# Performance work log

Hardware: AMD Instinct MI355X
Metric: run time of the kernel (lower is better)

## Reference

```python
import jax, jax.numpy as jnp
import numpy as np

B, N, C_IN, C_OUT, F = 8, 2048, 256, 256, 8
EPS = 1e-4

def setup_inputs() -> dict:
    key = jax.random.key(0)
    k1, k2, k3, k4, k5 = jax.random.split(key, 5)
    node_feats = jax.random.normal(k1, (B, N, C_IN), dtype=jnp.float32)
    # sparse-ish 0/1 adjacency with self-loops already added (as module assumes)
    adj = (jax.random.uniform(k2, (B, N, N)) < 0.02).astype(jnp.float32)
    eye = jnp.eye(N, dtype=jnp.float32)[None, :, :]
    adj_matrix = jnp.maximum(adj, eye)
    filters = jax.random.normal(k3, (F, C_OUT, C_IN), dtype=jnp.float32) * (1.0 / np.sqrt(C_IN))
    proj_w = jax.random.normal(k4, (1, F), dtype=jnp.float32) * (1.0 / np.sqrt(F))
    proj_b = jax.random.normal(k5, (1,), dtype=jnp.float32) * 0.01
    return {"node_feats": node_feats, "adj_matrix": adj_matrix,
            "filters": filters, "proj_w": proj_w, "proj_b": proj_b}

def reference(node_feats, adj_matrix, filters, proj_w, proj_b):
    # Multi-head filter transform + projection over heads, fused algebraically:
    # torch: ext[b,n,k,f] = sum_i filters[f,k,i]*x[b,n,i]; x' = ext @ proj_w.T + proj_b
    x = jnp.einsum('bni,fki,f->bnk', node_feats, filters, proj_w[0]) + proj_b[0]  # [B,N,c_out]
    # adjacency-weighted aggregation + mean normalization
    num_neighbours = jnp.sum(adj_matrix, axis=-1, keepdims=True)  # [B,N,1]
    agg = jnp.einsum('bij,bjk->bik', adj_matrix, x)  # [B,N,c_out]
    return agg / (num_neighbours + EPS)
```

## Files before the change

kernel.cpp:

```cpp
#include <hip/hip_runtime.h>
#include <hip/hip_bf16.h>

#define B_DIM  8
#define N_DIM  2048
#define CIN    256
#define COUT   256
#define F_DIM  8
#define EPS    1e-4f

using short8 = __attribute__((ext_vector_type(8))) short;
using f32x4  = __attribute__((ext_vector_type(4))) float;

__device__ __forceinline__ unsigned short f2bf(float f) {
    union { float f; unsigned u; } x; x.f = f;
    unsigned r = x.u + 0x7FFFu + ((x.u >> 16) & 1u);
    return (unsigned short)(r >> 16);
}
__device__ __forceinline__ float bf2f(unsigned short u) {
    union { unsigned u; float f; } x; x.u = ((unsigned)u) << 16;
    return x.f;
}

__global__ __launch_bounds__(256) void wb_build(const float* __restrict__ filters,
                                                const float* __restrict__ proj_w,
                                                unsigned short* __restrict__ Wb) {
    int gid = blockIdx.x * 256 + threadIdx.x;
    float acc = 0.f;
#pragma unroll
    for (int f = 0; f < F_DIM; ++f)
        acc += proj_w[f] * filters[f * (COUT * CIN) + gid];
    Wb[gid] = f2bf(acc);
}

__global__ __launch_bounds__(256) void xp_gemm(const float* __restrict__ nf,
                                               const unsigned short* __restrict__ Wb,
                                               const float* __restrict__ proj_b,
                                               unsigned short* __restrict__ xp) {
    const int tid  = threadIdx.x;
    const int lane = tid & 63;
    const int wv   = tid >> 6;
    const int m0   = blockIdx.x * 64;
    const int lrow = lane & 15;
    const int kgrp = lane >> 4;
    const float bias = proj_b[0];

    f32x4 acc[4][4];
#pragma unroll
    for (int a = 0; a < 4; ++a)
#pragma unroll
        for (int b = 0; b < 4; ++b)
            acc[a][b] = (f32x4){0.f, 0.f, 0.f, 0.f};

#pragma unroll
    for (int ks = 0; ks < 8; ++ks) {
        const int klane = ks * 32 + kgrp * 8;
        short8 af[4], bfr[4];
#pragma unroll
        for (int fm = 0; fm < 4; ++fm) {
            const float* ap = nf + (size_t)(m0 + fm * 16 + lrow) * CIN + klane;
            float4 a0 = *(const float4*)ap;
            float4 a1 = *(const float4*)(ap + 4);
            short8 t;
            t[0] = (short)f2bf(a0.x); t[1] = (short)f2bf(a0.y);
            t[2] = (short)f2bf(a0.z); t[3] = (short)f2bf(a0.w);
            t[4] = (short)f2bf(a1.x); t[5] = (short)f2bf(a1.y);
            t[6] = (short)f2bf(a1.z); t[7] = (short)f2bf(a1.w);
            af[fm] = t;
        }
#pragma unroll
        for (int fn = 0; fn < 4; ++fn) {
            const unsigned short* bp =
                Wb + (size_t)(wv * 64 + fn * 16 + lrow) * CIN + klane;
            bfr[fn] = *(const short8*)bp;
        }
#pragma unroll
        for (int fm = 0; fm < 4; ++fm)
#pragma unroll
            for (int fn = 0; fn < 4; ++fn)
                acc[fm][fn] = __builtin_amdgcn_mfma_f32_16x16x32_bf16(
                    af[fm], bfr[fn], acc[fm][fn], 0, 0, 0);
    }

#pragma unroll
    for (int fm = 0; fm < 4; ++fm) {
#pragma unroll
        for (int fn = 0; fn < 4; ++fn) {
            const int gcol = wv * 64 + fn * 16 + lrow;
#pragma unroll
            for (int r = 0; r < 4; ++r) {
                const int grow = m0 + fm * 16 + kgrp * 4 + r;
                xp[(size_t)grow * COUT + gcol] = f2bf(acc[fm][fn][r] + bias);
            }
        }
    }
}

__global__ __launch_bounds__(256) void agg_sparse(const float* __restrict__ adj,
                                                  const unsigned short* __restrict__ xp,
                                                  float* __restrict__ out) {
    __shared__ int   s_idx[N_DIM];
    __shared__ float s_val[N_DIM];
    __shared__ int   s_wcnt[4];
    __shared__ float s_wdeg[4];

    const int tid  = threadIdx.x;
    const int lane = tid & 63;
    const int wid  = tid >> 6;
    const int bid  = blockIdx.x;
    const int b    = bid & 7;
    const int i    = bid >> 3;

    const float* row = adj + ((size_t)b * N_DIM + i) * N_DIM;

    const float4* r4 = (const float4*)(row + tid * 8);
    float4 va = r4[0], vb = r4[1];
    float v[8] = {va.x, va.y, va.z, va.w, vb.x, vb.y, vb.z, vb.w};

    int   c = 0;
    float dsum = 0.f;
#pragma unroll
    for (int e = 0; e < 8; ++e) { dsum += v[e]; c += (v[e] != 0.f); }

    int pre = c;
#pragma unroll
    for (int off = 1; off < 64; off <<= 1) {
        int n = __shfl_up(pre, off, 64);
        if (lane >= off) pre += n;
    }
    float ds = dsum;
#pragma unroll
    for (int off = 32; off; off >>= 1) ds += __shfl_down(ds, off, 64);
    if (lane == 63) s_wcnt[wid] = pre;
    if (lane == 0)  s_wdeg[wid] = ds;
    __syncthreads();

    int base = 0;
#pragma unroll
    for (int ww = 0; ww < 4; ++ww) if (ww < wid) base += s_wcnt[ww];
    const int   cnt = s_wcnt[0] + s_wcnt[1] + s_wcnt[2] + s_wcnt[3];
    const float deg = s_wdeg[0] + s_wdeg[1] + s_wdeg[2] + s_wdeg[3];

    int p = base + (pre - c);
#pragma unroll
    for (int e = 0; e < 8; ++e) {
        if (v[e] != 0.f) { s_idx[p] = tid * 8 + e; s_val[p] = v[e]; ++p; }
    }
    __syncthreads();

    const unsigned short* xb = xp + (size_t)b * N_DIM * COUT + tid;
    float acc = 0.f;
    int t = 0;
    for (; t + 4 <= cnt; t += 4) {
        int j0 = s_idx[t], j1 = s_idx[t + 1], j2 = s_idx[t + 2], j3 = s_idx[t + 3];
        float w0 = s_val[t], w1 = s_val[t + 1], w2 = s_val[t + 2], w3 = s_val[t + 3];
        float x0 = bf2f(xb[(size_t)j0 * COUT]);
        float x1 = bf2f(xb[(size_t)j1 * COUT]);
        float x2 = bf2f(xb[(size_t)j2 * COUT]);
        float x3 = bf2f(xb[(size_t)j3 * COUT]);
        acc += w0 * x0; acc += w1 * x1; acc += w2 * x2; acc += w3 * x3;
    }
    for (; t < cnt; ++t)
        acc += s_val[t] * bf2f(xb[(size_t)s_idx[t] * COUT]);

    out[((size_t)b * N_DIM + i) * COUT + tid] = acc / (deg + EPS);
}

extern "C" void kernel_launch(void* const* d_in, const int* in_sizes, int n_in,
                              void* d_out, int out_size, void* d_ws, size_t ws_size,
                              hipStream_t stream) {
    const float* nf      = (const float*)d_in[0];
    const float* adj     = (const float*)d_in[1];
    const float* filters = (const float*)d_in[2];
    const float* proj_w  = (const float*)d_in[3];
    const float* proj_b  = (const float*)d_in[4];
    float* out = (float*)d_out;

    unsigned short* Wb = (unsigned short*)d_ws;
    unsigned short* xp = (unsigned short*)((char*)d_ws + COUT * CIN * 2);

    wb_build<<<(COUT * CIN) / 256, 256, 0, stream>>>(filters, proj_w, Wb);
    xp_gemm<<<(B_DIM * N_DIM) / 64, 256, 0, stream>>>(nf, Wb, proj_b, xp);
    agg_sparse<<<B_DIM * N_DIM, 256, 0, stream>>>(adj, xp, out);
}
```

Baseline: 73.98 us.

## Replace sparse gather aggregation with dense bf16 MFMA adjacency GEMM

The sparse per-row compaction and gather is replaced by a dense MFMA GEMM that multiplies the adjacency (truncated to bf16, exact for 0/1 values) by a transposed projected feature matrix, computing degrees on the fly. The feature GEMM is reoriented to write x' transposed so B-operand loads are contiguous. This removes the irregular gathers and shared-memory compaction, but performs dense work and launches only 256 blocks, which may limit memory-level parallelism when streaming the large adjacency. Truncating adjacency to bf16 assumes exactly representable values.

```diff
diff --git a/kernel.cpp b/kernel.cpp
--- a/kernel.cpp
+++ b/kernel.cpp
@@ -7,6 +7,7 @@
 #define COUT   256
 #define F_DIM  8
 #define EPS    1e-4f
+#define MTOT   (B_DIM * N_DIM)
 
 using short8 = __attribute__((ext_vector_type(8))) short;
 using f32x4  = __attribute__((ext_vector_type(4))) float;
@@ -16,9 +17,9 @@
     unsigned r = x.u + 0x7FFFu + ((x.u >> 16) & 1u);
     return (unsigned short)(r >> 16);
 }
-__device__ __forceinline__ float bf2f(unsigned short u) {
-    union { unsigned u; float f; } x; x.u = ((unsigned)u) << 16;
-    return x.f;
+__device__ __forceinline__ unsigned fbits(float f) {
+    union { float f; unsigned u; } x; x.f = f;
+    return x.u;
 }
 
 __global__ __launch_bounds__(256) void wb_build(const float* __restrict__ filters,
@@ -32,16 +33,17 @@
     Wb[gid] = f2bf(acc);
 }
 
-__global__ __launch_bounds__(256) void xp_gemm(const float* __restrict__ nf,
-                                               const unsigned short* __restrict__ Wb,
-                                               const float* __restrict__ proj_b,
-                                               unsigned short* __restrict__ xp) {
+__global__ __launch_bounds__(256) void xpT_gemm(const float* __restrict__ nf,
+                                                const unsigned short* __restrict__ Wb,
+                                                const float* __restrict__ proj_b,
+                                                unsigned short* __restrict__ xpT) {
     const int tid  = threadIdx.x;
     const int lane = tid & 63;
     const int wv   = tid >> 6;
-    const int m0   = blockIdx.x * 64;
     const int lrow = lane & 15;
     const int kgrp = lane >> 4;
+    const int m0   = (blockIdx.x & 3) * 64;
+    const int n0   = (blockIdx.x >> 2) * 256 + wv * 64;
     const float bias = proj_b[0];
 
     f32x4 acc[4][4];
@@ -56,22 +58,19 @@
         const int klane = ks * 32 + kgrp * 8;
         short8 af[4], bfr[4];
 #pragma unroll
-        for (int fm = 0; fm < 4; ++fm) {
-            const float* ap = nf + (size_t)(m0 + fm * 16 + lrow) * CIN + klane;
-            float4 a0 = *(const float4*)ap;
-            float4 a1 = *(const float4*)(ap + 4);
+        for (int fm = 0; fm < 4; ++fm)
+            af[fm] = *(const short8*)&Wb[(size_t)(m0 + fm * 16 + lrow) * CIN + klane];
+#pragma unroll
+        for (int fn = 0; fn < 4; ++fn) {
+            const float* bp = nf + (size_t)(n0 + fn * 16 + lrow) * CIN + klane;
+            float4 b0 = *(const float4*)bp;
+            float4 b1 = *(const float4*)(bp + 4);
             short8 t;
-            t[0] = (short)f2bf(a0.x); t[1] = (short)f2bf(a0.y);
-            t[2] = (short)f2bf(a0.z); t[3] = (short)f2bf(a0.w);
-            t[4] = (short)f2bf(a1.x); t[5] = (short)f2bf(a1.y);
-            t[6] = (short)f2bf(a1.z); t[7] = (short)f2bf(a1.w);
-            af[fm] = t;
-        }
-#pragma unroll
-        for (int fn = 0; fn < 4; ++fn) {
-            const unsigned short* bp =
-                Wb + (size_t)(wv * 64 + fn * 16 + lrow) * CIN + klane;
-            bfr[fn] = *(const short8*)bp;
+            t[0] = (short)f2bf(b0.x); t[1] = (short)f2bf(b0.y);
+            t[2] = (short)f2bf(b0.z); t[3] = (short)f2bf(b0.w);
+            t[4] = (short)f2bf(b1.x); t[5] = (short)f2bf(b1.y);
+            t[6] = (short)f2bf(b1.z); t[7] = (short)f2bf(b1.w);
+            bfr[fn] = t;
         }
 #pragma unroll
         for (int fm = 0; fm < 4; ++fm)
@@ -82,87 +81,127 @@
     }
 
 #pragma unroll
-    for (int fm = 0; fm < 4; ++fm) {
+    for (int fm = 0; fm < 4; ++fm)
 #pragma unroll
         for (int fn = 0; fn < 4; ++fn) {
-            const int gcol = wv * 64 + fn * 16 + lrow;
+            const int g = n0 + fn * 16 + lrow;
 #pragma unroll
             for (int r = 0; r < 4; ++r) {
-                const int grow = m0 + fm * 16 + kgrp * 4 + r;
-                xp[(size_t)grow * COUT + gcol] = f2bf(acc[fm][fn][r] + bias);
+                const int c = m0 + fm * 16 + kgrp * 4 + r;
+                xpT[(size_t)c * MTOT + g] = f2bf(acc[fm][fn][r] + bias);
             }
         }
-    }
-}
-
-__global__ __launch_bounds__(256) void agg_sparse(const float* __restrict__ adj,
-                                                  const unsigned short* __restrict__ xp,
-                                                  float* __restrict__ out) {
-    __shared__ int   s_idx[N_DIM];
-    __shared__ float s_val[N_DIM];
-    __shared__ int   s_wcnt[4];
-    __shared__ float s_wdeg[4];
-
+}
+
+#define COMPUTE_STEP(AR, BR)                                                     \
+    {                                                                            \
+        short8 af_[4];                                                           \
+        _Pragma("unroll")                                                        \
+        for (int fm = 0; fm < 4; ++fm) {                                         \
+            float4 x0 = AR[fm][0], x1 = AR[fm][1];                               \
+            deg[fm] += x0.x + x0.y + x0.z + x0.w + x1.x + x1.y + x1.z + x1.w;    \
+            short8 t;                                                            \
+            t[0] = (short)(fbits(x0.x) >> 16); t[1] = (short)(fbits(x0.y) >> 16);\
+            t[2] = (short)(fbits(x0.z) >> 16); t[3] = (short)(fbits(x0.w) >> 16);\
+            t[4] = (short)(fbits(x1.x) >> 16); t[5] = (short)(fbits(x1.y) >> 16);\
+            t[6] = (short)(fbits(x1.z) >> 16); t[7] = (short)(fbits(x1.w) >> 16);\
+            af_[fm] = t;                                                         \
+        }                                                                        \
+        _Pragma("unroll")                                                        \
+        for (int fm = 0; fm < 4; ++fm)                                           \
+            _Pragma("unroll")                                                    \
+            for (int fn = 0; fn < 4; ++fn)                                       \
+                acc[fm][fn] = __builtin_amdgcn_mfma_f32_16x16x32_bf16(           \
+                    af_[fm], BR[fn], acc[fm][fn], 0, 0, 0);                      \
+    }
+
+__global__ __launch_bounds__(256) void adj_gemm(const float* __restrict__ adj,
+                                                const unsigned short* __restrict__ xpT,
+                                                float* __restrict__ out) {
     const int tid  = threadIdx.x;
     const int lane = tid & 63;
-    const int wid  = tid >> 6;
+    const int wv   = tid >> 6;
+    const int lrow = lane & 15;
+    const int kgrp = lane >> 4;
     const int bid  = blockIdx.x;
     const int b    = bid & 7;
-    const int i    = bid >> 3;
-
-    const float* row = adj + ((size_t)b * N_DIM + i) * N_DIM;
-
-    const float4* r4 = (const float4*)(row + tid * 8);
-    float4 va = r4[0], vb = r4[1];
-    float v[8] = {va.x, va.y, va.z, va.w, vb.x, vb.y, vb.z, vb.w};
-
-    int   c = 0;
-    float dsum = 0.f;
-#pragma unroll
-    for (int e = 0; e < 8; ++e) { dsum += v[e]; c += (v[e] != 0.f); }
-
-    int pre = c;
-#pragma unroll
-    for (int off = 1; off < 64; off <<= 1) {
-        int n = __shfl_up(pre, off, 64);
-        if (lane >= off) pre += n;
-    }
-    float ds = dsum;
-#pragma unroll
-    for (int off = 32; off; off >>= 1) ds += __shfl_down(ds, off, 64);
-    if (lane == 63) s_wcnt[wid] = pre;
-    if (lane == 0)  s_wdeg[wid] = ds;
-    __syncthreads();
-
-    int base = 0;
-#pragma unroll
-    for (int ww = 0; ww < 4; ++ww) if (ww < wid) base += s_wcnt[ww];
-    const int   cnt = s_wcnt[0] + s_wcnt[1] + s_wcnt[2] + s_wcnt[3];
-    const float deg = s_wdeg[0] + s_wdeg[1] + s_wdeg[2] + s_wdeg[3];
-
-    int p = base + (pre - c);
-#pragma unroll
-    for (int e = 0; e < 8; ++e) {
-        if (v[e] != 0.f) { s_idx[p] = tid * 8 + e; s_val[p] = v[e]; ++p; }
-    }
-    __syncthreads();
-
-    const unsigned short* xb = xp + (size_t)b * N_DIM * COUT + tid;
-    float acc = 0.f;
-    int t = 0;
-    for (; t + 4 <= cnt; t += 4) {
-        int j0 = s_idx[t], j1 = s_idx[t + 1], j2 = s_idx[t + 2], j3 = s_idx[t + 3];
-        float w0 = s_val[t], w1 = s_val[t + 1], w2 = s_val[t + 2], w3 = s_val[t + 3];
-        float x0 = bf2f(xb[(size_t)j0 * COUT]);
-        float x1 = bf2f(xb[(size_t)j1 * COUT]);
-        float x2 = bf2f(xb[(size_t)j2 * COUT]);
-        float x3 = bf2f(xb[(size_t)j3 * COUT]);
-        acc += w0 * x0; acc += w1 * x1; acc += w2 * x2; acc += w3 * x3;
-    }
-    for (; t < cnt; ++t)
-        acc += s_val[t] * bf2f(xb[(size_t)s_idx[t] * COUT]);
-
-    out[((size_t)b * N_DIM + i) * COUT + tid] = acc / (deg + EPS);
+    const int row0 = (bid >> 3) * 64;
+    const int n0   = wv * 64;
+
+    const float* aptr[4];
+#pragma unroll
+    for (int fm = 0; fm < 4; ++fm)
+        aptr[fm] = adj + ((size_t)b * N_DIM + row0 + fm * 16 + lrow) * N_DIM + kgrp * 8;
+    const unsigned short* bptr[4];
+#pragma unroll
+    for (int fn = 0; fn < 4; ++fn)
+        bptr[fn] = xpT + (size_t)(n0 + fn * 16 + lrow) * MTOT + b * N_DIM + kgrp * 8;
+
+    f32x4 acc[4][4];
+#pragma unroll
+    for (int a = 0; a < 4; ++a)
+#pragma unroll
+        for (int c = 0; c < 4; ++c)
+            acc[a][c] = (f32x4){0.f, 0.f, 0.f, 0.f};
+    float deg[4] = {0.f, 0.f, 0.f, 0.f};
+
+    float4 A0[4][2], A1[4][2];
+    short8 B0[4], B1[4];
+#pragma unroll
+    for (int fm = 0; fm < 4; ++fm) {
+        A0[fm][0] = *(const float4*)(aptr[fm]);
+        A0[fm][1] = *(const float4*)(aptr[fm] + 4);
+    }
+#pragma unroll
+    for (int fn = 0; fn < 4; ++fn)
+        B0[fn] = *(const short8*)(bptr[fn]);
+
+#pragma unroll 1
+    for (int t = 0; t < 32; ++t) {
+        const int j1 = t * 64 + 32;
+#pragma unroll
+        for (int fm = 0; fm < 4; ++fm) {
+            A1[fm][0] = *(const float4*)(aptr[fm] + j1);
+            A1[fm][1] = *(const float4*)(aptr[fm] + j1 + 4);
+        }
+#pragma unroll
+        for (int fn = 0; fn < 4; ++fn)
+            B1[fn] = *(const short8*)(bptr[fn] + j1);
+
+        COMPUTE_STEP(A0, B0);
+
+        const int j2 = (t < 31) ? t * 64 + 64 : 0;
+#pragma unroll
+        for (int fm = 0; fm < 4; ++fm) {
+            A0[fm][0] = *(const float4*)(aptr[fm] + j2);
+            A0[fm][1] = *(const float4*)(aptr[fm] + j2 + 4);
+        }
+#pragma unroll
+        for (int fn = 0; fn < 4; ++fn)
+            B0[fn] = *(const short8*)(bptr[fn] + j2);
+
+        COMPUTE_STEP(A1, B1);
+    }
+
+#pragma unroll
+    for (int fm = 0; fm < 4; ++fm) {
+        float d = deg[fm];
+        d += __shfl_xor(d, 16, 64);
+        d += __shfl_xor(d, 32, 64);
+        deg[fm] = d;
+    }
+
+#pragma unroll
+    for (int fm = 0; fm < 4; ++fm)
+#pragma unroll
+        for (int r = 0; r < 4; ++r) {
+            const float dv  = __shfl(deg[fm], kgrp * 4 + r, 64);
+            const float inv = __builtin_amdgcn_rcpf(dv + EPS);
+            const int grow  = b * N_DIM + row0 + fm * 16 + kgrp * 4 + r;
+#pragma unroll
+            for (int fn = 0; fn < 4; ++fn)
+                out[(size_t)grow * COUT + n0 + fn * 16 + lrow] = acc[fm][fn][r] * inv;
+        }
 }
 
 extern "C" void kernel_launch(void* const* d_in, const int* in_sizes, int n_in,
@@ -175,10 +214,10 @@
     const float* proj_b  = (const float*)d_in[4];
     float* out = (float*)d_out;
 
-    unsigned short* Wb = (unsigned short*)d_ws;
-    unsigned short* xp = (unsigned short*)((char*)d_ws + COUT * CIN * 2);
+    unsigned short* Wb  = (unsigned short*)d_ws;
+    unsigned short* xpT = (unsigned short*)((char*)d_ws + COUT * CIN * 2);
 
     wb_build<<<(COUT * CIN) / 256, 256, 0, stream>>>(filters, proj_w, Wb);
-    xp_gemm<<<(B_DIM * N_DIM) / 64, 256, 0, stream>>>(nf, Wb, proj_b, xp);
-    agg_sparse<<<B_DIM * N_DIM, 256, 0, stream>>>(adj, xp, out);
-}
+    xpT_gemm<<<256, 256, 0, stream>>>(nf, Wb, proj_b, xpT);
+    adj_gemm<<<256, 256, 0, stream>>>(adj, xpT, out);
+}
```

Measured after the change: 114.4 us. 1.55x slower.
